# Optimization experiments

Hardware: AMD Instinct MI355X
Metric: run time of the kernel (lower is better)

The kernel has to match this reference:

```python
import jax, jax.numpy as jnp
import numpy as np

HIDDEN = 1024
Q_OUT = 2048
KV_OUT = 1024
HEAD_DIM = 128
N_Q = Q_OUT // HEAD_DIM      # 16
N_KV = KV_OUT // HEAD_DIM    # 8
EPS = 1e-6
ROPE_BASE = 10000.0


def _rms_norm(x, w, eps=EPS):
    # normalize over last dim (head_dim)
    ms = jnp.mean(x * x, axis=-1, keepdims=True)
    return x * jax.lax.rsqrt(ms + eps) * w


def _rope_cos_sin(t, dim=HEAD_DIM, base=ROPE_BASE):
    inv_freq = 1.0 / (base ** (jnp.arange(0, dim, 2, dtype=jnp.float32) / dim))
    pos = jnp.arange(t, dtype=jnp.float32)
    freqs = pos[:, None] * inv_freq[None, :]          # (T, D/2)
    emb = jnp.concatenate([freqs, freqs], axis=-1)    # (T, D)
    return jnp.cos(emb), jnp.sin(emb)


def _rotate_half(x):
    d = x.shape[-1] // 2
    return jnp.concatenate([-x[..., d:], x[..., :d]], axis=-1)


def setup_inputs() -> dict:
    key = jax.random.key(0)
    ks = jax.random.split(key, 7)
    def lin(k, fan_in, fan_out):
        # nn.Linear default init: U(-1/sqrt(fan_in), 1/sqrt(fan_in)); stored as (in, out) for x @ W
        bound = 1.0 / np.sqrt(fan_in)
        return jax.random.uniform(k, (fan_in, fan_out), jnp.float32, -bound, bound)
    return {
        "x": jax.random.normal(ks[0], (2, 2048, HIDDEN), jnp.float32),
        "Wq": lin(ks[1], HIDDEN, Q_OUT),
        "Wk": lin(ks[2], HIDDEN, KV_OUT),
        "Wv": lin(ks[3], HIDDEN, KV_OUT),
        "Wo": lin(ks[4], Q_OUT, HIDDEN),
        "q_norm_w": jnp.ones((HEAD_DIM,), jnp.float32),
        "k_norm_w": jnp.ones((HEAD_DIM,), jnp.float32),
    }


def reference(x, Wq, Wk, Wv, Wo, q_norm_w, k_norm_w):
    b, t, _ = x.shape
    # QKV projections, shaped to (B, H, T, D)
    q = (x @ Wq).reshape(b, t, N_Q, HEAD_DIM).transpose(0, 2, 1, 3)
    k = (x @ Wk).reshape(b, t, N_KV, HEAD_DIM).transpose(0, 2, 1, 3)
    v = (x @ Wv).reshape(b, t, N_KV, HEAD_DIM).transpose(0, 2, 1, 3)
    # per-head RMSNorm on q/k
    q = _rms_norm(q, q_norm_w)
    k = _rms_norm(k, k_norm_w)
    # RoPE (positions 0..T-1)
    cos, sin = _rope_cos_sin(t)                        # (T, D)
    cos = cos[None, None]; sin = sin[None, None]       # (1,1,T,D)
    q = q * cos + _rotate_half(q) * sin
    k = k * cos + _rotate_half(k) * sin
    # GQA: repeat_interleave kv heads to match q heads
    rep = N_Q // N_KV
    k_r = jnp.repeat(k, rep, axis=1)                   # (B, Hq, T, D)
    v_r = jnp.repeat(v, rep, axis=1)
    # causal attention
    scores = jnp.einsum('bhqd,bhkd->bhqk', q, k_r) / jnp.sqrt(jnp.asarray(HEAD_DIM, x.dtype))
    causal = jnp.triu(jnp.full((t, t), -jnp.inf, dtype=scores.dtype), k=1)[None, None]
    attn = jax.nn.softmax(scores + causal, axis=-1)
    out = jnp.einsum('bhqk,bhkd->bhqd', attn, v_r)     # (B, Hq, T, D)
    out = out.transpose(0, 2, 1, 3).reshape(b, t, Q_OUT)
    return out @ Wo
```

## Files before the change

kernel.cpp:

```cpp
#include <hip/hip_runtime.h>
#include <math.h>

typedef __attribute__((ext_vector_type(8))) short short8;
typedef __attribute__((ext_vector_type(4))) float f32x4;
typedef __attribute__((ext_vector_type(4))) unsigned int uint4v;

#define HIDDEN 1024
#define QOUT 2048
#define KVOUT 1024
#define HD 128
#define TSEQ 2048

union U8 { uint4v u; short8 s; };

__device__ __forceinline__ float bf2f(unsigned short h) {
    union { unsigned int u; float f; } x; x.u = ((unsigned int)h) << 16; return x.f;
}
__device__ __forceinline__ unsigned short f2bf(float f) {
    union { float f; unsigned int u; } x; x.f = f;
    unsigned int r = (x.u + 0x7fffu + ((x.u >> 16) & 1u)) >> 16;
    return (unsigned short)r;
}
__device__ __forceinline__ unsigned int pk2bf(float lo, float hi) {
    return (unsigned int)f2bf(lo) | ((unsigned int)f2bf(hi) << 16);
}

__device__ __forceinline__ void glds16(const unsigned short* g, unsigned short* l) {
    __builtin_amdgcn_global_load_lds(
        (const __attribute__((address_space(1))) unsigned int*)g,
        (__attribute__((address_space(3))) unsigned int*)l, 16, 0, 0);
}

__global__ __launch_bounds__(256) void cast_f32_bf16(const float* __restrict__ in,
                                                     unsigned short* __restrict__ out, int n4) {
    int i = blockIdx.x * 256 + threadIdx.x;
    if (i >= n4) return;
    float4 v = *(const float4*)(in + (size_t)i * 4);
    unsigned short o[4] = {f2bf(v.x), f2bf(v.y), f2bf(v.z), f2bf(v.w)};
    *(unsigned long long*)(out + (size_t)i * 4) = *(unsigned long long*)o;
}

__global__ __launch_bounds__(256) void transpose_f32_bf16(const float* __restrict__ W,
                                                          unsigned short* __restrict__ Wt,
                                                          int K, int N) {
    __shared__ __attribute__((aligned(16))) unsigned short Ls[64 * 72];
    int ntiles = N >> 6;
    int kt = blockIdx.x / ntiles, nt = blockIdx.x - kt * ntiles;
    int k0 = kt * 64, n0 = nt * 64;
    int tid = threadIdx.x;
    for (int t = 0; t < 4; t++) {
        int idx = tid + t * 256;
        int r = idx >> 4, seg = idx & 15;
        float4 v = *(const float4*)(W + (size_t)(k0 + r) * N + n0 + seg * 4);
        int c = seg * 4;
        Ls[(c + 0) * 72 + r] = f2bf(v.x);
        Ls[(c + 1) * 72 + r] = f2bf(v.y);
        Ls[(c + 2) * 72 + r] = f2bf(v.z);
        Ls[(c + 3) * 72 + r] = f2bf(v.w);
    }
    __syncthreads();
    for (int t = 0; t < 2; t++) {
        int idx = tid + t * 256;
        int rr = idx >> 3, seg = idx & 7;
        uint4v v = *(const uint4v*)(Ls + rr * 72 + seg * 8);
        *(uint4v*)(Wt + (size_t)(n0 + rr) * K + k0 + seg * 8) = v;
    }
}

template <int OUT_BF16, int BN>
__global__ __launch_bounds__(256) void gemm_bt(const unsigned short* __restrict__ A,
                                               const unsigned short* __restrict__ Bt,
                                               void* __restrict__ Cout,
                                               int M, int N, int K) {
    constexpr int MT = (BN == 128) ? 4 : 2;
    __shared__ __attribute__((aligned(16))) unsigned short As[128 * 32];
    __shared__ __attribute__((aligned(16))) unsigned short Bs[BN * 32];
    const int tid = threadIdx.x;
    const int lane = tid & 63;
    const int warp = tid >> 6;
    const int ln = lane & 15;
    const int quad = lane >> 4;
    const int wm = (BN == 128) ? (warp >> 1) : warp;
    const int wn = (BN == 128) ? (warp & 1) : 0;
    const int m0 = blockIdx.y * 128;
    const int n0 = blockIdx.x * BN;

    const int srow = lane >> 2;
    const int schunk = (lane & 3) ^ (srow & 3);
    const unsigned short* Ag = A + (size_t)(m0 + warp * 16 + srow) * K + schunk * 8;
    const unsigned short* Bg = Bt + (size_t)(n0 + warp * 16 + srow) * K + schunk * 8;
    unsigned short* AsW = As + warp * 16 * 32;
    unsigned short* BsW = Bs + warp * 16 * 32;

    f32x4 acc[MT][4];
    for (int i = 0; i < MT; i++)
        for (int j = 0; j < 4; j++) acc[i][j] = (f32x4){0.f, 0.f, 0.f, 0.f};

    const int rq = quad ^ (ln & 3);
    for (int k0 = 0; k0 < K; k0 += 32) {
        __syncthreads();
        glds16(Ag + k0, AsW);
        glds16(Ag + (size_t)64 * K + k0, AsW + 64 * 32);
        glds16(Bg + k0, BsW);
        if (BN == 128) glds16(Bg + (size_t)64 * K + k0, BsW + 64 * 32);
        __syncthreads();
        short8 af[MT], bf[4];
        for (int mt = 0; mt < MT; mt++)
            af[mt] = *(const short8*)(As + (wm * (MT * 16) + mt * 16 + ln) * 32 + rq * 8);
        for (int nt = 0; nt < 4; nt++)
            bf[nt] = *(const short8*)(Bs + (wn * 64 + nt * 16 + ln) * 32 + rq * 8);
        for (int mt = 0; mt < MT; mt++)
            for (int nt = 0; nt < 4; nt++)
                acc[mt][nt] = __builtin_amdgcn_mfma_f32_16x16x32_bf16(af[mt], bf[nt], acc[mt][nt], 0, 0, 0);
    }
    for (int mt = 0; mt < MT; mt++)
        for (int nt = 0; nt < 4; nt++) {
            int col = n0 + wn * 64 + nt * 16 + ln;
            for (int r = 0; r < 4; r++) {
                int row = m0 + wm * (MT * 16) + mt * 16 + quad * 4 + r;
                float v = acc[mt][nt][r];
                if (OUT_BF16)
                    ((unsigned short*)Cout)[(size_t)row * N + col] = f2bf(v);
                else
                    ((float*)Cout)[(size_t)row * N + col] = v;
            }
        }
}

__global__ __launch_bounds__(256) void norm_rope(const unsigned short* __restrict__ QKV,
                                                 const float* __restrict__ qw,
                                                 const float* __restrict__ kw,
                                                 unsigned short* __restrict__ Q,
                                                 unsigned short* __restrict__ Kb) {
    int warp = threadIdx.x >> 6;
    int lane = threadIdx.x & 63;
    int gid = blockIdx.x * 4 + warp;
    int tok = gid / 24;
    int slot = gid - tok * 24;
    int b = tok >> 11, t = tok & 2047;
    const float* w;
    unsigned short* dst;
    int col0;
    if (slot < 16) {
        col0 = slot * HD;
        dst = Q + ((size_t)(b * 16 + slot) * TSEQ + t) * HD;
        w = qw;
    } else {
        int hk = slot - 16;
        col0 = QOUT + hk * HD;
        dst = Kb + ((size_t)(b * 8 + hk) * TSEQ + t) * HD;
        w = kw;
    }
    const unsigned short* row = QKV + (size_t)tok * 4096 + col0;
    float e0 = bf2f(row[lane]), e1 = bf2f(row[lane + 64]);
    float ss = e0 * e0 + e1 * e1;
    for (int off = 1; off < 64; off <<= 1) ss += __shfl_xor(ss, off);
    float rr = rsqrtf(ss * (1.0f / 128.0f) + 1e-6f);
    float n0 = e0 * rr * w[lane];
    float n1 = e1 * rr * w[lane + 64];
    float invf = __builtin_exp2f(-(float)lane * 0.20762050593045951f);
    float ang = (float)t * invf;
    float sf, cf;
    __sincosf(ang, &sf, &cf);
    float o0 = n0 * cf - n1 * sf;
    float o1 = n1 * cf + n0 * sf;
    dst[lane] = f2bf(o0);
    dst[lane + 64] = f2bf(o1);
}

__global__ __launch_bounds__(256) void v_transpose(const unsigned short* __restrict__ QKV,
                                                   unsigned short* __restrict__ Vt) {
    __shared__ __attribute__((aligned(16))) unsigned short Ls[128 * 72];
    int bid = blockIdx.x;
    int tt = bid & 31, hk = (bid >> 5) & 7, b = bid >> 8;
    int t0 = tt * 64;
    int tid = threadIdx.x;
    const unsigned short* base = QKV + (size_t)(b * 2048 + t0) * 4096 + 3072 + hk * 128;
    for (int i = 0; i < 4; i++) {
        int idx = tid + i * 256;
        int r = idx >> 4, seg = idx & 15;
        uint4v v = *(const uint4v*)(base + (size_t)r * 4096 + seg * 8);
        unsigned short* pv = (unsigned short*)&v;
        int d = seg * 8;
        for (int jj = 0; jj < 8; jj++) Ls[(d + jj) * 72 + r] = pv[jj];
    }
    __syncthreads();
    unsigned short* out = Vt + (size_t)(b * 8 + hk) * 128 * 2048;
    for (int i = 0; i < 4; i++) {
        int idx = tid + i * 256;
        int d = idx >> 3, seg = idx & 7;
        uint4v v = *(const uint4v*)(Ls + d * 72 + seg * 8);
        *(uint4v*)(out + (size_t)d * 2048 + t0 + seg * 8) = v;
    }
}

__global__ __launch_bounds__(256, 2) void attn(const unsigned short* __restrict__ Q,
                                               const unsigned short* __restrict__ Kg,
                                               const unsigned short* __restrict__ Vt,
                                               unsigned short* __restrict__ Og) {
    __shared__ __attribute__((aligned(16))) unsigned short Ks[64 * 128];
    __shared__ __attribute__((aligned(16))) unsigned short Vs[128 * 64];
    const int p = blockIdx.x;
    const int bh = blockIdx.y;
    const int b = bh >> 4, h = bh & 15, hk = h >> 1;
    const int tid = threadIdx.x;
    const int warp = tid >> 6, lane = tid & 63, ln = lane & 15, quad = lane >> 4;
    const int strip[2] = { p * 64 + warp * 16, (31 - p) * 64 + warp * 16 };
    const int jdiag[2] = { p, 31 - p };

    const unsigned short* Kbase = Kg + (size_t)(b * 8 + hk) * TSEQ * HD;
    const unsigned short* Vbase = Vt + (size_t)(b * 8 + hk) * HD * TSEQ;
    const unsigned short* Qh = Q + (size_t)(b * 16 + h) * TSEQ * HD;

    short8 qf[2][4];
    for (int st = 0; st < 2; st++)
        for (int kt = 0; kt < 4; kt++)
            qf[st][kt] = *(const short8*)(Qh + (size_t)(strip[st] + ln) * HD + kt * 32 + quad * 8);

    f32x4 o[2][8];
    for (int st = 0; st < 2; st++)
        for (int ot = 0; ot < 8; ot++) o[st][ot] = (f32x4){0.f, 0.f, 0.f, 0.f};
    float m_[2] = {-1e30f, -1e30f}, l_[2] = {0.f, 0.f};

    const int kr = lane >> 4;
    const int kc = lane & 15;
    const int vr = lane >> 3;
    const int vc = lane & 7;
    const int baseq = (quad & 1) * 2;
    const int i0 = ln + 16 * baseq;
    const int i1 = ln + 16 * (baseq + 1);
    const bool qlow = quad < 2;

    const float kscale = 0.12750580997495268f;
    const int nT = 32 - p;
    for (int j = 0; j < nT; j++) {
        const int j0 = j * 64;
        __syncthreads();
        for (int c = 0; c < 4; c++) {
            int row = warp * 16 + c * 4 + kr;
            glds16(Kbase + (size_t)(j0 + row) * HD + ((kc ^ (row & 15)) * 8),
                   Ks + (warp * 16 + c * 4) * 128);
        }
        for (int c = 0; c < 4; c++) {
            int d = warp * 32 + c * 8 + vr;
            glds16(Vbase + (size_t)d * TSEQ + j0 + ((vc ^ (d & 7)) * 8),
                   Vs + (warp * 32 + c * 8) * 64);
        }
        __syncthreads();
        for (int st = 0; st < 2; st++) {
            if (j > jdiag[st]) continue;
            f32x4 s[4];
            for (int kb = 0; kb < 4; kb++) s[kb] = (f32x4){0.f, 0.f, 0.f, 0.f};
            for (int kt = 0; kt < 4; kt++)
                for (int kb = 0; kb < 4; kb++) {
                    short8 kf = *(const short8*)(Ks + (kb * 16 + ln) * 128 + (((kt * 4 + quad) ^ ln) * 8));
                    s[kb] = __builtin_amdgcn_mfma_f32_16x16x32_bf16(kf, qf[st][kt], s[kb], 0, 0, 0);
                }
            float mx = -1e30f;
            if (j == jdiag[st]) {
                const int qloc = warp * 16 + ln;
                for (int kb = 0; kb < 4; kb++)
                    for (int r = 0; r < 4; r++) {
                        int kvloc = kb * 16 + quad * 4 + r;
                        float v = s[kb][r] * kscale;
                        v = (kvloc > qloc) ? -1e30f : v;
                        s[kb][r] = v;
                        mx = fmaxf(mx, v);
                    }
            } else {
                for (int kb = 0; kb < 4; kb++)
                    for (int r = 0; r < 4; r++) {
                        float v = s[kb][r] * kscale;
                        s[kb][r] = v;
                        mx = fmaxf(mx, v);
                    }
            }
            mx = fmaxf(mx, __shfl_xor(mx, 16));
            mx = fmaxf(mx, __shfl_xor(mx, 32));
            float mn = fmaxf(m_[st], mx);
            float al = __builtin_exp2f(m_[st] - mn);
            float sum = 0.f;
            for (int kb = 0; kb < 4; kb++)
                for (int r = 0; r < 4; r++) {
                    float pv = __builtin_exp2f(s[kb][r] - mn);
                    s[kb][r] = pv;
                    sum += pv;
                }
            sum += __shfl_xor(sum, 16);
            sum += __shfl_xor(sum, 32);
            m_[st] = mn;
            l_[st] = l_[st] * al + sum;
            unsigned int P2[4][2];
            for (int kb = 0; kb < 4; kb++) {
                P2[kb][0] = pk2bf(s[kb][0], s[kb][1]);
                P2[kb][1] = pk2bf(s[kb][2], s[kb][3]);
            }
            U8 pf0, pf1;
            {
                unsigned a, bb;
                a = __shfl(P2[0][0], i0); bb = __shfl(P2[1][0], i0); pf0.u[0] = qlow ? a : bb;
                a = __shfl(P2[0][1], i0); bb = __shfl(P2[1][1], i0); pf0.u[1] = qlow ? a : bb;
                a = __shfl(P2[0][0], i1); bb = __shfl(P2[1][0], i1); pf0.u[2] = qlow ? a : bb;
                a = __shfl(P2[0][1], i1); bb = __shfl(P2[1][1], i1); pf0.u[3] = qlow ? a : bb;
                a = __shfl(P2[2][0], i0); bb = __shfl(P2[3][0], i0); pf1.u[0] = qlow ? a : bb;
                a = __shfl(P2[2][1], i0); bb = __shfl(P2[3][1], i0); pf1.u[1] = qlow ? a : bb;
                a = __shfl(P2[2][0], i1); bb = __shfl(P2[3][0], i1); pf1.u[2] = qlow ? a : bb;
                a = __shfl(P2[2][1], i1); bb = __shfl(P2[3][1], i1); pf1.u[3] = qlow ? a : bb;
            }
            if (__any(al != 1.0f)) {
                float a4[4];
                for (int r = 0; r < 4; r++) a4[r] = __shfl(al, quad * 4 + r);
                for (int ot = 0; ot < 8; ot++)
                    for (int r = 0; r < 4; r++) o[st][ot][r] *= a4[r];
            }
            for (int ot = 0; ot < 8; ot++) {
                short8 vf0 = *(const short8*)(Vs + (ot * 16 + ln) * 64 + ((quad ^ (ln & 7)) * 8));
                short8 vf1 = *(const short8*)(Vs + (ot * 16 + ln) * 64 + (((4 + quad) ^ (ln & 7)) * 8));
                o[st][ot] = __builtin_amdgcn_mfma_f32_16x16x32_bf16(pf0.s, vf0, o[st][ot], 0, 0, 0);
                o[st][ot] = __builtin_amdgcn_mfma_f32_16x16x32_bf16(pf1.s, vf1, o[st][ot], 0, 0, 0);
            }
        }
    }
    for (int st = 0; st < 2; st++) {
        float inv[4];
        for (int r = 0; r < 4; r++) inv[r] = 1.0f / __shfl(l_[st], quad * 4 + r);
        for (int ot = 0; ot < 8; ot++) {
            int col = h * 128 + ot * 16 + ln;
            for (int r = 0; r < 4; r++) {
                int row = strip[st] + quad * 4 + r;
                Og[((size_t)(b * TSEQ + row)) * QOUT + col] = f2bf(o[st][ot][r] * inv[r]);
            }
        }
    }
}

extern "C" void kernel_launch(void* const* d_in, const int* in_sizes, int n_in,
                              void* d_out, int out_size, void* d_ws, size_t ws_size,
                              hipStream_t stream) {
    (void)in_sizes; (void)n_in; (void)out_size;
    const float* x  = (const float*)d_in[0];
    const float* Wq = (const float*)d_in[1];
    const float* Wk = (const float*)d_in[2];
    const float* Wv = (const float*)d_in[3];
    const float* Wo = (const float*)d_in[4];
    const float* qw = (const float*)d_in[5];
    const float* kw = (const float*)d_in[6];

    char* ws = (char*)d_ws;
    const size_t MB = 1024 * 1024;
    unsigned short* Wt   = (unsigned short*)(ws);
    unsigned short* Wot  = (unsigned short*)(ws + 8 * MB);
    unsigned short* QKVb = (unsigned short*)(ws + 12 * MB);
    unsigned short* xb   = (unsigned short*)(ws + 44 * MB);
    unsigned short* Qb   = (unsigned short*)(ws + 52 * MB);
    unsigned short* Kb   = (unsigned short*)(ws + 68 * MB);
    unsigned short* Vtb  = (unsigned short*)(ws + 76 * MB);
    unsigned short* Ob   = (unsigned short*)(ws + 84 * MB);
    if (ws_size < 100 * MB) return;

    cast_f32_bf16<<<dim3(4096), 256, 0, stream>>>(x, xb, 1048576);
    transpose_f32_bf16<<<dim3(512), 256, 0, stream>>>(Wq, Wt, 1024, 2048);
    transpose_f32_bf16<<<dim3(256), 256, 0, stream>>>(Wk, Wt + (size_t)2048 * 1024, 1024, 1024);
    transpose_f32_bf16<<<dim3(256), 256, 0, stream>>>(Wv, Wt + (size_t)3072 * 1024, 1024, 1024);
    transpose_f32_bf16<<<dim3(512), 256, 0, stream>>>(Wo, Wot, 2048, 1024);
    gemm_bt<1, 128><<<dim3(32, 32), 256, 0, stream>>>(xb, Wt, QKVb, 4096, 4096, 1024);
    norm_rope<<<dim3(24576), 256, 0, stream>>>(QKVb, qw, kw, Qb, Kb);
    v_transpose<<<dim3(512), 256, 0, stream>>>(QKVb, Vtb);
    attn<<<dim3(16, 32), 256, 0, stream>>>(Qb, Kb, Vtb, Ob);
    gemm_bt<0, 64><<<dim3(16, 32), 256, 0, stream>>>(Ob, Wot, (float*)d_out, 4096, 1024, 2048);
}
```

Before: 300.5 us.

## Transpose MFMA operand order for vectorized stores and LDS-based P exchange in attention

The GEMM swaps the MFMA A/B operands so each lane holds four consecutive output columns, which allows packed 8-byte bf16 or 16-byte fp32 stores instead of scalar stores. In attention, the two query strips are merged into one pass that shares K fragment loads and V fragment loads between strips. The cross-lane shuffles that rearranged P are replaced by a per-warp LDS staging buffer. The transposed layout also removes the shuffles for alpha and l, and makes the output stores vectorized. The cost is extra LDS traffic and registers for two score sets at once, which may lower occupancy.

```diff
diff --git a/kernel.cpp b/kernel.cpp
--- a/kernel.cpp
+++ b/kernel.cpp
@@ -10,8 +10,6 @@
 #define KVOUT 1024
 #define HD 128
 #define TSEQ 2048
-
-union U8 { uint4v u; short8 s; };
 
 __device__ __forceinline__ float bf2f(unsigned short h) {
     union { unsigned int u; float f; } x; x.u = ((unsigned int)h) << 16; return x.f;
@@ -111,20 +109,22 @@
             bf[nt] = *(const short8*)(Bs + (wn * 64 + nt * 16 + ln) * 32 + rq * 8);
         for (int mt = 0; mt < MT; mt++)
             for (int nt = 0; nt < 4; nt++)
-                acc[mt][nt] = __builtin_amdgcn_mfma_f32_16x16x32_bf16(af[mt], bf[nt], acc[mt][nt], 0, 0, 0);
-    }
-    for (int mt = 0; mt < MT; mt++)
+                acc[mt][nt] = __builtin_amdgcn_mfma_f32_16x16x32_bf16(bf[nt], af[mt], acc[mt][nt], 0, 0, 0);
+    }
+    for (int mt = 0; mt < MT; mt++) {
+        int row = m0 + wm * (MT * 16) + mt * 16 + ln;
         for (int nt = 0; nt < 4; nt++) {
-            int col = n0 + wn * 64 + nt * 16 + ln;
-            for (int r = 0; r < 4; r++) {
-                int row = m0 + wm * (MT * 16) + mt * 16 + quad * 4 + r;
-                float v = acc[mt][nt][r];
-                if (OUT_BF16)
-                    ((unsigned short*)Cout)[(size_t)row * N + col] = f2bf(v);
-                else
-                    ((float*)Cout)[(size_t)row * N + col] = v;
+            int colb = n0 + wn * 64 + nt * 16 + quad * 4;
+            if (OUT_BF16) {
+                unsigned long long pk =
+                    (unsigned long long)pk2bf(acc[mt][nt][0], acc[mt][nt][1]) |
+                    ((unsigned long long)pk2bf(acc[mt][nt][2], acc[mt][nt][3]) << 32);
+                *(unsigned long long*)((unsigned short*)Cout + (size_t)row * N + colb) = pk;
+            } else {
+                *(f32x4*)((float*)Cout + (size_t)row * N + colb) = acc[mt][nt];
             }
         }
+    }
 }
 
 __global__ __launch_bounds__(256) void norm_rope(const unsigned short* __restrict__ QKV,
@@ -200,6 +200,7 @@
                                                unsigned short* __restrict__ Og) {
     __shared__ __attribute__((aligned(16))) unsigned short Ks[64 * 128];
     __shared__ __attribute__((aligned(16))) unsigned short Vs[128 * 64];
+    __shared__ __attribute__((aligned(16))) unsigned short Ps[4][16 * 72];
     const int p = blockIdx.x;
     const int bh = blockIdx.y;
     const int b = bh >> 4, h = bh & 15, hk = h >> 1;
@@ -226,10 +227,6 @@
     const int kc = lane & 15;
     const int vr = lane >> 3;
     const int vc = lane & 7;
-    const int baseq = (quad & 1) * 2;
-    const int i0 = ln + 16 * baseq;
-    const int i1 = ln + 16 * (baseq + 1);
-    const bool qlow = quad < 2;
 
     const float kscale = 0.12750580997495268f;
     const int nT = 32 - p;
@@ -247,89 +244,93 @@
                    Vs + (warp * 32 + c * 8) * 64);
         }
         __syncthreads();
-        for (int st = 0; st < 2; st++) {
-            if (j > jdiag[st]) continue;
-            f32x4 s[4];
-            for (int kb = 0; kb < 4; kb++) s[kb] = (f32x4){0.f, 0.f, 0.f, 0.f};
-            for (int kt = 0; kt < 4; kt++)
-                for (int kb = 0; kb < 4; kb++) {
-                    short8 kf = *(const short8*)(Ks + (kb * 16 + ln) * 128 + (((kt * 4 + quad) ^ ln) * 8));
-                    s[kb] = __builtin_amdgcn_mfma_f32_16x16x32_bf16(kf, qf[st][kt], s[kb], 0, 0, 0);
-                }
+        const bool act0 = (j <= jdiag[0]);
+        f32x4 s[2][4];
+        for (int kb = 0; kb < 4; kb++) {
+            s[0][kb] = (f32x4){0.f, 0.f, 0.f, 0.f};
+            s[1][kb] = (f32x4){0.f, 0.f, 0.f, 0.f};
+        }
+        for (int kt = 0; kt < 4; kt++) {
+            short8 kf[4];
+            for (int kb = 0; kb < 4; kb++)
+                kf[kb] = *(const short8*)(Ks + (kb * 16 + ln) * 128 + (((kt * 4 + quad) ^ ln) * 8));
+            for (int kb = 0; kb < 4; kb++)
+                s[1][kb] = __builtin_amdgcn_mfma_f32_16x16x32_bf16(kf[kb], qf[1][kt], s[1][kb], 0, 0, 0);
+            if (act0)
+                for (int kb = 0; kb < 4; kb++)
+                    s[0][kb] = __builtin_amdgcn_mfma_f32_16x16x32_bf16(kf[kb], qf[0][kt], s[0][kb], 0, 0, 0);
+        }
+        short8 pf[2][2];
+        float al[2] = {1.f, 1.f};
+        for (int st = (act0 ? 0 : 1); st < 2; st++) {
             float mx = -1e30f;
             if (j == jdiag[st]) {
                 const int qloc = warp * 16 + ln;
                 for (int kb = 0; kb < 4; kb++)
                     for (int r = 0; r < 4; r++) {
                         int kvloc = kb * 16 + quad * 4 + r;
-                        float v = s[kb][r] * kscale;
+                        float v = s[st][kb][r] * kscale;
                         v = (kvloc > qloc) ? -1e30f : v;
-                        s[kb][r] = v;
+                        s[st][kb][r] = v;
                         mx = fmaxf(mx, v);
                     }
             } else {
                 for (int kb = 0; kb < 4; kb++)
                     for (int r = 0; r < 4; r++) {
-                        float v = s[kb][r] * kscale;
-                        s[kb][r] = v;
+                        float v = s[st][kb][r] * kscale;
+                        s[st][kb][r] = v;
                         mx = fmaxf(mx, v);
                     }
             }
             mx = fmaxf(mx, __shfl_xor(mx, 16));
             mx = fmaxf(mx, __shfl_xor(mx, 32));
             float mn = fmaxf(m_[st], mx);
-            float al = __builtin_exp2f(m_[st] - mn);
+            al[st] = __builtin_exp2f(m_[st] - mn);
             float sum = 0.f;
             for (int kb = 0; kb < 4; kb++)
                 for (int r = 0; r < 4; r++) {
-                    float pv = __builtin_exp2f(s[kb][r] - mn);
-                    s[kb][r] = pv;
+                    float pv = __builtin_exp2f(s[st][kb][r] - mn);
+                    s[st][kb][r] = pv;
                     sum += pv;
                 }
             sum += __shfl_xor(sum, 16);
             sum += __shfl_xor(sum, 32);
             m_[st] = mn;
-            l_[st] = l_[st] * al + sum;
-            unsigned int P2[4][2];
+            l_[st] = l_[st] * al[st] + sum;
             for (int kb = 0; kb < 4; kb++) {
-                P2[kb][0] = pk2bf(s[kb][0], s[kb][1]);
-                P2[kb][1] = pk2bf(s[kb][2], s[kb][3]);
+                unsigned long long pk =
+                    (unsigned long long)pk2bf(s[st][kb][0], s[st][kb][1]) |
+                    ((unsigned long long)pk2bf(s[st][kb][2], s[st][kb][3]) << 32);
+                *(unsigned long long*)(&Ps[warp][ln * 72 + kb * 16 + quad * 4]) = pk;
             }
-            U8 pf0, pf1;
-            {
-                unsigned a, bb;
-                a = __shfl(P2[0][0], i0); bb = __shfl(P2[1][0], i0); pf0.u[0] = qlow ? a : bb;
-                a = __shfl(P2[0][1], i0); bb = __shfl(P2[1][1], i0); pf0.u[1] = qlow ? a : bb;
-                a = __shfl(P2[0][0], i1); bb = __shfl(P2[1][0], i1); pf0.u[2] = qlow ? a : bb;
-                a = __shfl(P2[0][1], i1); bb = __shfl(P2[1][1], i1); pf0.u[3] = qlow ? a : bb;
-                a = __shfl(P2[2][0], i0); bb = __shfl(P2[3][0], i0); pf1.u[0] = qlow ? a : bb;
-                a = __shfl(P2[2][1], i0); bb = __shfl(P2[3][1], i0); pf1.u[1] = qlow ? a : bb;
-                a = __shfl(P2[2][0], i1); bb = __shfl(P2[3][0], i1); pf1.u[2] = qlow ? a : bb;
-                a = __shfl(P2[2][1], i1); bb = __shfl(P2[3][1], i1); pf1.u[3] = qlow ? a : bb;
+            pf[st][0] = *(const short8*)(&Ps[warp][ln * 72 + quad * 8]);
+            pf[st][1] = *(const short8*)(&Ps[warp][ln * 72 + 32 + quad * 8]);
+        }
+        if (act0 && __any(al[0] != 1.0f))
+            for (int ot = 0; ot < 8; ot++)
+                for (int r = 0; r < 4; r++) o[0][ot][r] *= al[0];
+        if (__any(al[1] != 1.0f))
+            for (int ot = 0; ot < 8; ot++)
+                for (int r = 0; r < 4; r++) o[1][ot][r] *= al[1];
+        for (int ot = 0; ot < 8; ot++) {
+            short8 vf0 = *(const short8*)(Vs + (ot * 16 + ln) * 64 + ((quad ^ (ln & 7)) * 8));
+            short8 vf1 = *(const short8*)(Vs + (ot * 16 + ln) * 64 + (((4 + quad) ^ (ln & 7)) * 8));
+            o[1][ot] = __builtin_amdgcn_mfma_f32_16x16x32_bf16(vf0, pf[1][0], o[1][ot], 0, 0, 0);
+            o[1][ot] = __builtin_amdgcn_mfma_f32_16x16x32_bf16(vf1, pf[1][1], o[1][ot], 0, 0, 0);
+            if (act0) {
+                o[0][ot] = __builtin_amdgcn_mfma_f32_16x16x32_bf16(vf0, pf[0][0], o[0][ot], 0, 0, 0);
+                o[0][ot] = __builtin_amdgcn_mfma_f32_16x16x32_bf16(vf1, pf[0][1], o[0][ot], 0, 0, 0);
             }
-            if (__any(al != 1.0f)) {
-                float a4[4];
-                for (int r = 0; r < 4; r++) a4[r] = __shfl(al, quad * 4 + r);
-                for (int ot = 0; ot < 8; ot++)
-                    for (int r = 0; r < 4; r++) o[st][ot][r] *= a4[r];
-            }
-            for (int ot = 0; ot < 8; ot++) {
-                short8 vf0 = *(const short8*)(Vs + (ot * 16 + ln) * 64 + ((quad ^ (ln & 7)) * 8));
-                short8 vf1 = *(const short8*)(Vs + (ot * 16 + ln) * 64 + (((4 + quad) ^ (ln & 7)) * 8));
-                o[st][ot] = __builtin_amdgcn_mfma_f32_16x16x32_bf16(pf0.s, vf0, o[st][ot], 0, 0, 0);
-                o[st][ot] = __builtin_amdgcn_mfma_f32_16x16x32_bf16(pf1.s, vf1, o[st][ot], 0, 0, 0);
-            }
         }
     }
     for (int st = 0; st < 2; st++) {
-        float inv[4];
-        for (int r = 0; r < 4; r++) inv[r] = 1.0f / __shfl(l_[st], quad * 4 + r);
+        float inv = 1.0f / l_[st];
+        size_t rowoff = ((size_t)(b * TSEQ + strip[st] + ln)) * QOUT + h * 128 + quad * 4;
         for (int ot = 0; ot < 8; ot++) {
-            int col = h * 128 + ot * 16 + ln;
-            for (int r = 0; r < 4; r++) {
-                int row = strip[st] + quad * 4 + r;
-                Og[((size_t)(b * TSEQ + row)) * QOUT + col] = f2bf(o[st][ot][r] * inv[r]);
-            }
+            unsigned long long pk =
+                (unsigned long long)pk2bf(o[st][ot][0] * inv, o[st][ot][1] * inv) |
+                ((unsigned long long)pk2bf(o[st][ot][2] * inv, o[st][ot][3] * inv) << 32);
+            *(unsigned long long*)(Og + rowoff + ot * 16) = pk;
         }
     }
 }
```

Result: slower. 535.7 us (+78.3%).
